# Optimization experiments

Hardware: AMD Instinct MI355X
Metric: run time of the kernel (lower is better)

## Reference

```python
import jax, jax.numpy as jnp
import numpy as np
import math

VOCAB, D, L, H, DFF, S, B = 32000, 1024, 6, 16, 4096, 512, 4
DK = D // H
EPS = 1e-6


def layernorm(x, g, b):
    # Faithful to source: divides by (std + eps), std is population std (unbiased=False)
    mu = jnp.mean(x, axis=-1, keepdims=True)
    std = jnp.sqrt(jnp.mean((x - mu) ** 2, axis=-1, keepdims=True))
    return g * (x - mu) / (std + EPS) + b


def setup_inputs() -> dict:
    key = jax.random.key(0)
    ks = jax.random.split(key, 12)
    s = 0.02
    inp = {
        "tokens": jax.random.randint(ks[0], (B, S), 0, VOCAB, dtype=jnp.int32),
        "tok_emb": jax.random.normal(ks[1], (VOCAB, D), jnp.float32) * s,
        "pos_emb": jax.random.normal(ks[2], (1, S, D), jnp.float32) * s,
        # per-layer stacked params [L, ...]
        "Wq": jax.random.normal(ks[3], (L, D, D), jnp.float32) * s,
        "bq": jnp.zeros((L, D), jnp.float32),
        "Wk": jax.random.normal(ks[4], (L, D, D), jnp.float32) * s,
        "bk": jnp.zeros((L, D), jnp.float32),
        "Wv": jax.random.normal(ks[5], (L, D, D), jnp.float32) * s,
        "bv": jnp.zeros((L, D), jnp.float32),
        "Wo": jax.random.normal(ks[6], (L, D, D), jnp.float32) * s,
        "bo": jnp.zeros((L, D), jnp.float32),
        "g1": jnp.ones((L, D), jnp.float32),
        "be1": jnp.zeros((L, D), jnp.float32),
        "W1": jax.random.normal(ks[7], (L, D, DFF), jnp.float32) * s,
        "bf1": jnp.zeros((L, DFF), jnp.float32),
        "W2": jax.random.normal(ks[8], (L, DFF, D), jnp.float32) * s,
        "bf2": jnp.zeros((L, D), jnp.float32),
        "g2": jnp.ones((L, D), jnp.float32),
        "be2": jnp.zeros((L, D), jnp.float32),
        "gf": jnp.ones((D,), jnp.float32),
        "bf": jnp.zeros((D,), jnp.float32),
    }
    return inp


def gpt_forward(tokens, tok_emb, pos_emb, Wq, bq, Wk, bk, Wv, bv, Wo, bo,
                g1, be1, W1, bf1, W2, bf2, g2, be2, gf, bf):
    seq = tokens.shape[1]
    x = tok_emb[tokens] * math.sqrt(D) + pos_emb[:, :seq, :]  # [B,S,D]
    causal = jnp.tril(jnp.ones((seq, seq), bool))  # [S,S]

    def block(x, p):
        wq, bq_, wk, bk_, wv, bv_, wo, bo_, g1_, be1_, w1, bf1_, w2, bf2_, g2_, be2_ = p
        h = layernorm(x, g1_, be1_)
        q = (h @ wq + bq_).reshape(B, seq, H, DK).transpose(0, 2, 1, 3)  # [B,H,S,DK]
        k = (h @ wk + bk_).reshape(B, seq, H, DK).transpose(0, 2, 1, 3)
        v = (h @ wv + bv_).reshape(B, seq, H, DK).transpose(0, 2, 1, 3)
        scores = jnp.einsum("bhqd,bhkd->bhqk", q, k) / math.sqrt(DK)
        scores = jnp.where(causal, scores, -1e9)
        p_attn = jax.nn.softmax(scores, axis=-1)
        attn = jnp.einsum("bhqk,bhkd->bhqd", p_attn, v)
        attn = attn.transpose(0, 2, 1, 3).reshape(B, seq, D)
        x = x + (attn @ wo + bo_)
        h2 = layernorm(x, g2_, be2_)
        ff = jnp.maximum(h2 @ w1 + bf1_, 0.0) @ w2 + bf2_
        return x + ff, None

    params = (Wq, bq, Wk, bk, Wv, bv, Wo, bo, g1, be1, W1, bf1, W2, bf2, g2, be2)
    x, _ = jax.lax.scan(block, x, params)
    x = layernorm(x, gf, bf)
    logits = x @ tok_emb.T  # tied head, no bias
    return logits


def reference(tokens, tok_emb, pos_emb, Wq, bq, Wk, bk, Wv, bv, Wo, bo,
              g1, be1, W1, bf1, W2, bf2, g2, be2, gf, bf):
    return gpt_forward(tokens, tok_emb, pos_emb, Wq, bq, Wk, bk, Wv, bv, Wo, bo,
                       g1, be1, W1, bf1, W2, bf2, g2, be2, gf, bf)
```

## Files before the change

### kernel.cpp

```cpp
#include <hip/hip_runtime.h>

#define TOKENS 2048
#define DM 1024
#define NHEAD 16
#define DH 64
#define SEQL 512
#define NBATCH 4
#define DFFN 4096
#define NLAYER 6
#define NVOCAB 32000

typedef short short8 __attribute__((ext_vector_type(8)));
typedef short short4v __attribute__((ext_vector_type(4)));
typedef float floatx4 __attribute__((ext_vector_type(4)));

#define FLAG_RELU 1
#define FLAG_OUTBF16 2

#define AS1 __attribute__((address_space(1)))
#define AS3 __attribute__((address_space(3)))

__device__ __forceinline__ float bf2f(short s) {
  unsigned u = ((unsigned)(unsigned short)s) << 16;
  return __builtin_bit_cast(float, u);
}
__device__ __forceinline__ short f2bf(float f) {
  unsigned u = __builtin_bit_cast(unsigned, f);
  u = (u + 0x7FFFu + ((u >> 16) & 1u)) >> 16;
  return (short)(unsigned short)u;
}

template<int N> __device__ __forceinline__ void wait_vm() {
  if constexpr (N == 0)      asm volatile("s_waitcnt vmcnt(0)" ::: "memory");
  else if constexpr (N == 3) asm volatile("s_waitcnt vmcnt(3)" ::: "memory");
  else if constexpr (N == 4) asm volatile("s_waitcnt vmcnt(4)" ::: "memory");
  else if constexpr (N == 6) asm volatile("s_waitcnt vmcnt(6)" ::: "memory");
  else if constexpr (N == 8) asm volatile("s_waitcnt vmcnt(8)" ::: "memory");
  else static_assert(N == 0, "unsupported vmcnt");
}

template<int BM, int BN, int WR, int WC, int BK>
__global__ __launch_bounds__(256) void gemm_db(
    const short* __restrict__ A, const short* __restrict__ Bt, void* __restrict__ Cv,
    const float* __restrict__ bias, const float* __restrict__ resid,
    int K, int lda, int ldb, int ldc, float alpha, int flags)
{
  constexpr int FI = BM / WR / 16;
  constexpr int FJ = BN / WC / 16;
  constexpr int RPI = (BK == 64) ? 32 : 64;
  constexpr int NST = BM / RPI + BN / RPI;
  __shared__ short As[2][BM * BK];
  __shared__ short Bs[2][BN * BK];

  const int gy = gridDim.y;
  int lin = blockIdx.x + gridDim.x * blockIdx.y;
  const int nwg = gridDim.x * gy;
  if ((nwg & 7) == 0) { const int cpx = nwg >> 3; lin = (lin & 7) * cpx + (lin >> 3); }
  const int row0 = (lin % gy) * BM, col0 = (lin / gy) * BN;

  const int tid = threadIdx.x;
  const int lane = tid & 63;
  const int wid = tid >> 6;
  const int wr = wid / WC, wc = wid % WC;
  const int lc = lane & 15, g = lane >> 4;
  const int sr = (BK == 64) ? (tid >> 3) : (tid >> 2);
  const int sc = (BK == 64) ? (tid & 7) : (tid & 3);
  const int swz_s = (BK == 64) ? (sr & 7) : ((sr >> 1) & 3);
  const int scs = (sc ^ swz_s) * 8;

  floatx4 acc[FI][FJ];
  #pragma unroll
  for (int i = 0; i < FI; ++i)
    #pragma unroll
    for (int j = 0; j < FJ; ++j)
      acc[i][j] = (floatx4){0.f, 0.f, 0.f, 0.f};

  auto stage = [&](int k0, int b) {
    char* ad = (char*)As[b];
    char* bd = (char*)Bs[b];
    #pragma unroll
    for (int it = 0; it < BM / RPI; ++it) {
      const short* src = A + (long)(row0 + it * RPI + sr) * lda + k0 + scs;
      __builtin_amdgcn_global_load_lds((const AS1 void*)src,
          (AS3 void*)(ad + it * 4096 + tid * 16), 16, 0, 0);
    }
    #pragma unroll
    for (int it = 0; it < BN / RPI; ++it) {
      const short* src = Bt + (long)(col0 + it * RPI + sr) * ldb + k0 + scs;
      __builtin_amdgcn_global_load_lds((const AS1 void*)src,
          (AS3 void*)(bd + it * 4096 + tid * 16), 16, 0, 0);
    }
  };

  const int NT = K / BK;
  stage(0, 0);
  int cb = 0;
  for (int t = 0; t < NT; ++t) {
    __builtin_amdgcn_s_barrier();
    __builtin_amdgcn_sched_barrier(0);
    if (t + 1 < NT) {
      stage((t + 1) * BK, cb ^ 1);
      wait_vm<NST>();
    } else {
      wait_vm<0>();
    }
    __builtin_amdgcn_sched_barrier(0);

    const short* as = As[cb];
    const short* bs = Bs[cb];
    if constexpr (BK == 64) {
      short8 fa[FI][2], fb[FJ][2];
      #pragma unroll
      for (int i = 0; i < FI; ++i) {
        const int r = wr * (BM / WR) + i * 16 + lc;
        fa[i][0] = *(const short8*)&as[r * 64 + ((g ^ (r & 7)) * 8)];
        fa[i][1] = *(const short8*)&as[r * 64 + (((4 + g) ^ (r & 7)) * 8)];
      }
      #pragma unroll
      for (int j = 0; j < FJ; ++j) {
        const int r = wc * (BN / WC) + j * 16 + lc;
        fb[j][0] = *(const short8*)&bs[r * 64 + ((g ^ (r & 7)) * 8)];
        fb[j][1] = *(const short8*)&bs[r * 64 + (((4 + g) ^ (r & 7)) * 8)];
      }
      #pragma unroll
      for (int i = 0; i < FI; ++i)
        #pragma unroll
        for (int j = 0; j < FJ; ++j) {
          acc[i][j] = __builtin_amdgcn_mfma_f32_16x16x32_bf16(fa[i][0], fb[j][0], acc[i][j], 0, 0, 0);
          acc[i][j] = __builtin_amdgcn_mfma_f32_16x16x32_bf16(fa[i][1], fb[j][1], acc[i][j], 0, 0, 0);
        }
    } else {
      short8 fa[FI], fb[FJ];
      #pragma unroll
      for (int i = 0; i < FI; ++i) {
        const int r = wr * (BM / WR) + i * 16 + lc;
        fa[i] = *(const short8*)&as[r * 32 + ((g ^ ((r >> 1) & 3)) * 8)];
      }
      #pragma unroll
      for (int j = 0; j < FJ; ++j) {
        const int r = wc * (BN / WC) + j * 16 + lc;
        fb[j] = *(const short8*)&bs[r * 32 + ((g ^ ((r >> 1) & 3)) * 8)];
      }
      #pragma unroll
      for (int i = 0; i < FI; ++i)
        #pragma unroll
        for (int j = 0; j < FJ; ++j)
          acc[i][j] = __builtin_amdgcn_mfma_f32_16x16x32_bf16(fa[i], fb[j], acc[i][j], 0, 0, 0);
    }
    cb ^= 1;
  }

  const bool relu = flags & FLAG_RELU;
  const bool obf  = flags & FLAG_OUTBF16;
  float* Cf = (float*)Cv;
  short* Cb = (short*)Cv;
  #pragma unroll
  for (int i = 0; i < FI; ++i) {
    int orow = row0 + wr * (BM / WR) + i * 16 + g * 4;
    #pragma unroll
    for (int j = 0; j < FJ; ++j) {
      int ocol = col0 + wc * (BN / WC) + j * 16 + lc;
      #pragma unroll
      for (int t = 0; t < 4; ++t) {
        long off = (long)(orow + t) * ldc + ocol;
        float v = alpha * acc[i][j][t];
        if (bias)  v += bias[ocol];
        if (resid) v += resid[off];
        if (relu)  v = fmaxf(v, 0.f);
        if (obf) Cb[off] = f2bf(v); else Cf[off] = v;
      }
    }
  }
}

template<int BM, int BN, int WR, int WC, int BK>
static inline void launch_gemm(hipStream_t st, const short* A, const short* Bt, void* C,
    const float* bias, const float* resid, int M, int N, int K,
    int lda, int ldb, int ldc, float alpha, int flags)
{
  dim3 grid(N / BN, M / BM, 1), blk(256);
  gemm_db<BM, BN, WR, WC, BK><<<grid, blk, 0, st>>>(A, Bt, C, bias, resid,
                                                    K, lda, ldb, ldc, alpha, flags);
}

__global__ __launch_bounds__(512, 2) void gemm256h(
    const short* __restrict__ A, const short* __restrict__ Bt, float* __restrict__ C,
    int K, int lda, int ldb, int ldc)
{
  __shared__ short As[2][256 * 32];
  __shared__ short Bs[2][256 * 32];

  const int gy = gridDim.y;
  int lin = blockIdx.x + gridDim.x * blockIdx.y;
  const int nwg = gridDim.x * gy;
  if ((nwg & 7) == 0) { const int cpx = nwg >> 3; lin = (lin & 7) * cpx + (lin >> 3); }
  const int row0 = (lin % gy) * 256, col0 = (lin / gy) * 256;

  const int tid = threadIdx.x;
  const int lane = tid & 63;
  const int w = tid >> 6;
  const int wr = w >> 2, wc = w & 3;
  const int lc = lane & 15, g = lane >> 4;
  const int sr = tid >> 2;
  const int sc = tid & 3;
  const int scs = (sc ^ ((sr >> 1) & 3)) * 8;

  floatx4 acc[8][4];
  #pragma unroll
  for (int i = 0; i < 8; ++i)
    #pragma unroll
    for (int j = 0; j < 4; ++j)
      acc[i][j] = (floatx4){0.f, 0.f, 0.f, 0.f};

  auto stage = [&](int k0, int b) {
    char* ad = (char*)As[b];
    char* bd = (char*)Bs[b];
    #pragma unroll
    for (int it = 0; it < 2; ++it) {
      const short* src = A + (long)(row0 + it * 128 + sr) * lda + k0 + scs;
      __builtin_amdgcn_global_load_lds((const AS1 void*)src,
          (AS3 void*)(ad + it * 8192 + tid * 16), 16, 0, 0);
    }
    #pragma unroll
    for (int it = 0; it < 2; ++it) {
      const short* src = Bt + (long)(col0 + it * 128 + sr) * ldb + k0 + scs;
      __builtin_amdgcn_global_load_lds((const AS1 void*)src,
          (AS3 void*)(bd + it * 8192 + tid * 16), 16, 0, 0);
    }
  };

  const int NT = K >> 5;
  stage(0, 0);
  int cb = 0;
  for (int t = 0; t < NT; ++t) {
    __builtin_amdgcn_s_barrier();
    __builtin_amdgcn_sched_barrier(0);
    if (t + 1 < NT) {
      stage((t + 1) << 5, cb ^ 1);
      wait_vm<4>();
    } else {
      wait_vm<0>();
    }
    __builtin_amdgcn_sched_barrier(0);

    const short* as = As[cb];
    const short* bs = Bs[cb];
    short8 fa[8], fb[4];
    #pragma unroll
    for (int i = 0; i < 8; ++i) {
      const int r = wr * 128 + i * 16 + lc;
      fa[i] = *(const short8*)&as[r * 32 + ((g ^ ((r >> 1) & 3)) * 8)];
    }
    #pragma unroll
    for (int j = 0; j < 4; ++j) {
      const int r = wc * 64 + j * 16 + lc;
      fb[j] = *(const short8*)&bs[r * 32 + ((g ^ ((r >> 1) & 3)) * 8)];
    }
    #pragma unroll
    for (int i = 0; i < 8; ++i)
      #pragma unroll
      for (int j = 0; j < 4; ++j)
        acc[i][j] = __builtin_amdgcn_mfma_f32_16x16x32_bf16(fa[i], fb[j], acc[i][j], 0, 0, 0);
    cb ^= 1;
  }

  #pragma unroll
  for (int i = 0; i < 8; ++i) {
    int orow = row0 + wr * 128 + i * 16 + g * 4;
    #pragma unroll
    for (int j = 0; j < 4; ++j) {
      int ocol = col0 + wc * 64 + j * 16 + lc;
      #pragma unroll
      for (int t = 0; t < 4; ++t)
        C[(long)(orow + t) * ldc + ocol] = acc[i][j][t];
    }
  }
}

__global__ __launch_bounds__(256) void flash_attn(
    const short* __restrict__ qkv, const short* __restrict__ Vt,
    short* __restrict__ attn)
{
  const int qt = blockIdx.x;
  const int bh = blockIdx.y;
  const int b = bh >> 4, h = bh & 15;
  const int row0 = qt * 64;

  __shared__ short Kt[64 * 64];
  __shared__ short Vtl[64 * 64];
  __shared__ short Pt[4 * 16 * 64];

  const int tid = threadIdx.x;
  const int lane = tid & 63;
  const int wid = tid >> 6;
  const int lc = lane & 15, g = lane >> 4;

  short8 qf[2];
  {
    const short* qp = qkv + (long)(b * SEQL + row0 + wid * 16 + lc) * 3072 + h * DH;
    qf[0] = *(const short8*)(qp + g * 8);
    qf[1] = *(const short8*)(qp + 32 + g * 8);
  }

  floatx4 o[4];
  float m[4], l[4];
  #pragma unroll
  for (int j = 0; j < 4; ++j) o[j] = (floatx4){0.f, 0.f, 0.f, 0.f};
  #pragma unroll
  for (int t = 0; t < 4; ++t) { m[t] = -3e38f; l[t] = 0.f; }

  for (int kv0 = 0; kv0 <= row0; kv0 += 64) {
    #pragma unroll
    for (int i = 0; i < 2; ++i) {
      const int idx = i * 256 + tid;
      const int r = idx >> 3, cc = idx & 7;
      const int sw = cc ^ (r & 7);
      const short* ks = qkv + (long)(b * SEQL + kv0 + r) * 3072 + 1024 + h * DH + sw * 8;
      __builtin_amdgcn_global_load_lds((const AS1 void*)ks,
          (AS3 void*)((char*)Kt + (i * 256 + wid * 64) * 16), 16, 0, 0);
      const short* vs = Vt + (long)bh * DH * SEQL + (long)r * SEQL + kv0 + sw * 8;
      __builtin_amdgcn_global_load_lds((const AS1 void*)vs,
          (AS3 void*)((char*)Vtl + (i * 256 + wid * 64) * 16), 16, 0, 0);
    }
    __syncthreads();

    floatx4 s[4];
    #pragma unroll
    for (int j = 0; j < 4; ++j) s[j] = (floatx4){0.f, 0.f, 0.f, 0.f};
    #pragma unroll
    for (int ks_ = 0; ks_ < 2; ++ks_) {
      #pragma unroll
      for (int j = 0; j < 4; ++j) {
        const int row = j * 16 + lc;
        const short8 kf = *(const short8*)&Kt[row * 64 + ((ks_ * 4 + g) ^ (row & 7)) * 8];
        s[j] = __builtin_amdgcn_mfma_f32_16x16x32_bf16(qf[ks_], kf, s[j], 0, 0, 0);
      }
    }

    const bool diag = (kv0 == row0);
    float p[4][4], rmax[4], rsum[4], fs[4];
    #pragma unroll
    for (int t = 0; t < 4; ++t) rmax[t] = -3e38f;
    #pragma unroll
    for (int j = 0; j < 4; ++j)
      #pragma unroll
      for (int t = 0; t < 4; ++t) {
        float sv = s[j][t] * 0.125f;
        if (diag && (j * 16 + lc) > (wid * 16 + g * 4 + t)) sv = -3e38f;
        p[j][t] = sv;
        rmax[t] = fmaxf(rmax[t], sv);
      }
    #pragma unroll
    for (int t = 0; t < 4; ++t) {
      #pragma unroll
      for (int mk = 1; mk < 16; mk <<= 1)
        rmax[t] = fmaxf(rmax[t], __shfl_xor(rmax[t], mk));
      float mn = fmaxf(m[t], rmax[t]);
      fs[t] = __expf(m[t] - mn);
      m[t] = mn;
    }
    #pragma unroll
    for (int j = 0; j < 4; ++j)
      #pragma unroll
      for (int t = 0; t < 4; ++t)
        p[j][t] = __expf(p[j][t] - m[t]);
    #pragma unroll
    for (int t = 0; t < 4; ++t) {
      rsum[t] = p[0][t] + p[1][t] + p[2][t] + p[3][t];
      #pragma unroll
      for (int mk = 1; mk < 16; mk <<= 1)
        rsum[t] += __shfl_xor(rsum[t], mk);
      l[t] = l[t] * fs[t] + rsum[t];
    }
    #pragma unroll
    for (int j = 0; j < 4; ++j) {
      o[j][0] *= fs[0]; o[j][1] *= fs[1]; o[j][2] *= fs[2]; o[j][3] *= fs[3];
    }
    #pragma unroll
    for (int j = 0; j < 4; ++j)
      #pragma unroll
      for (int t = 0; t < 4; ++t) {
        const int r = g * 4 + t;
        const int col = j * 16 + lc;
        Pt[wid * 1024 + r * 64 + (((col >> 3) ^ (r & 7)) * 8) + (col & 7)] = f2bf(p[j][t]);
      }
    __syncthreads();

    #pragma unroll
    for (int ks_ = 0; ks_ < 2; ++ks_) {
      const short8 pf = *(const short8*)&Pt[wid * 1024 + lc * 64 + ((ks_ * 4 + g) ^ (lc & 7)) * 8];
      #pragma unroll
      for (int j = 0; j < 4; ++j) {
        const int row = j * 16 + lc;
        const short8 vf = *(const short8*)&Vtl[row * 64 + ((ks_ * 4 + g) ^ (row & 7)) * 8];
        o[j] = __builtin_amdgcn_mfma_f32_16x16x32_bf16(pf, vf, o[j], 0, 0, 0);
      }
    }
    __syncthreads();
  }

  float linv[4];
  #pragma unroll
  for (int t = 0; t < 4; ++t) linv[t] = 1.f / l[t];
  #pragma unroll
  for (int j = 0; j < 4; ++j)
    #pragma unroll
    for (int t = 0; t < 4; ++t) {
      const long row = (long)(b * SEQL + row0 + wid * 16 + g * 4 + t);
      attn[row * DM + h * DH + j * 16 + lc] = f2bf(o[j][t] * linv[t]);
    }
}

__global__ __launch_bounds__(256) void ln_bf16(const float* __restrict__ x,
    const float* __restrict__ gg, const float* __restrict__ bb, short* __restrict__ out)
{
  int row = blockIdx.x;
  const float4 u = ((const float4*)(x + (long)row * DM))[threadIdx.x];
  float s  = u.x + u.y + u.z + u.w;
  float sq = u.x * u.x + u.y * u.y + u.z * u.z + u.w * u.w;
  #pragma unroll
  for (int o = 32; o; o >>= 1) { s += __shfl_xor(s, o); sq += __shfl_xor(sq, o); }
  __shared__ float red[8];
  int lane = threadIdx.x & 63, wid = threadIdx.x >> 6;
  if (lane == 0) { red[wid] = s; red[4 + wid] = sq; }
  __syncthreads();
  s  = red[0] + red[1] + red[2] + red[3];
  sq = red[4] + red[5] + red[6] + red[7];
  float mu  = s * (1.f / DM);
  float var = fmaxf(sq * (1.f / DM) - mu * mu, 0.f);
  float inv = 1.f / (sqrtf(var) + 1e-6f);
  int c = threadIdx.x * 4;
  const float4 gv = ((const float4*)gg)[threadIdx.x];
  const float4 bv = ((const float4*)bb)[threadIdx.x];
  short4v o;
  o[0] = f2bf((u.x - mu) * inv * gv.x + bv.x);
  o[1] = f2bf((u.y - mu) * inv * gv.y + bv.y);
  o[2] = f2bf((u.z - mu) * inv * gv.z + bv.z);
  o[3] = f2bf((u.w - mu) * inv * gv.w + bv.w);
  *(short4v*)(out + (long)row * DM + c) = o;
}

__global__ __launch_bounds__(256) void embed_k(const int* __restrict__ toks,
    const float* __restrict__ emb, const float* __restrict__ pos, float* __restrict__ x)
{
  int row = blockIdx.x;
  int s = row & (SEQL - 1);
  long tk = toks[row];
  const float4 e = ((const float4*)(emb + tk * DM))[threadIdx.x];
  const float4 p = ((const float4*)(pos + (long)s * DM))[threadIdx.x];
  float4 o;
  o.x = e.x * 32.f + p.x; o.y = e.y * 32.f + p.y;
  o.z = e.z * 32.f + p.z; o.w = e.w * 32.f + p.w;
  ((float4*)(x + (long)row * DM))[threadIdx.x] = o;
}

__global__ void wtrans(const float* __restrict__ W, short* __restrict__ Wt,
                       int K, int N, long zsout)
{
  __shared__ float tile[32][33];
  const long lo = (long)blockIdx.z * K * N;
  const long oo = (long)blockIdx.z * zsout;
  int n0 = blockIdx.x * 32, k0 = blockIdx.y * 32;
  int tx = threadIdx.x, ty = threadIdx.y;
  #pragma unroll
  for (int i = 0; i < 4; ++i)
    tile[ty + i * 8][tx] = W[lo + (long)(k0 + ty + i * 8) * N + n0 + tx];
  __syncthreads();
  #pragma unroll
  for (int i = 0; i < 4; ++i)
    Wt[oo + (long)(n0 + ty + i * 8) * K + k0 + tx] = f2bf(tile[tx][ty + i * 8]);
}

__global__ __launch_bounds__(256) void conv_bf16(const float* __restrict__ in,
                                                 short* __restrict__ out)
{
  long i = ((long)blockIdx.x * 256 + threadIdx.x) * 8;
  float4 a = *(const float4*)(in + i);
  float4 b = *(const float4*)(in + i + 4);
  short8 o;
  o[0] = f2bf(a.x); o[1] = f2bf(a.y); o[2] = f2bf(a.z); o[3] = f2bf(a.w);
  o[4] = f2bf(b.x); o[5] = f2bf(b.y); o[6] = f2bf(b.z); o[7] = f2bf(b.w);
  *(short8*)(out + i) = o;
}

__global__ void vtrans(const short* __restrict__ qkv, short* __restrict__ Vt)
{
  __shared__ short tile[32][33];
  int bh = blockIdx.z;
  int b = bh >> 4, h = bh & 15;
  int s0 = blockIdx.x * 32, d0 = blockIdx.y * 32;
  int tx = threadIdx.x, ty = threadIdx.y;
  #pragma unroll
  for (int i = 0; i < 4; ++i)
    tile[ty + i * 8][tx] =
        qkv[((long)(b * SEQL + s0 + ty + i * 8)) * 3072 + 2048 + h * DH + d0 + tx];
  __syncthreads();
  #pragma unroll
  for (int i = 0; i < 4; ++i)
    Vt[((long)(bh * DH + d0 + ty + i * 8)) * SEQL + s0 + tx] = tile[tx][ty + i * 8];
}

__global__ void bias_cat(const float* __restrict__ bq, const float* __restrict__ bk,
                         const float* __restrict__ bv, float* __restrict__ out)
{
  int l = blockIdx.y;
  int i = blockIdx.x * 256 + threadIdx.x;
  float v = (i < 1024) ? bq[l * 1024 + i]
          : (i < 2048) ? bk[l * 1024 + i - 1024]
                       : bv[l * 1024 + i - 2048];
  out[(long)l * 3072 + i] = v;
}

extern "C" void kernel_launch(void* const* d_in, const int* in_sizes, int n_in,
                              void* d_out, int out_size, void* d_ws, size_t ws_size,
                              hipStream_t stream)
{
  (void)in_sizes; (void)n_in; (void)out_size;
  const int*   toks = (const int*)  d_in[0];
  const float* temb = (const float*)d_in[1];
  const float* pemb = (const float*)d_in[2];
  const float* Wq  = (const float*)d_in[3];  const float* bq  = (const float*)d_in[4];
  const float* Wk  = (const float*)d_in[5];  const float* bk  = (const float*)d_in[6];
  const float* Wv  = (const float*)d_in[7];  const float* bv  = (const float*)d_in[8];
  const float* Wo  = (const float*)d_in[9];  const float* bo  = (const float*)d_in[10];
  const float* g1  = (const float*)d_in[11]; const float* be1 = (const float*)d_in[12];
  const float* W1  = (const float*)d_in[13]; const float* bf1 = (const float*)d_in[14];
  const float* W2  = (const float*)d_in[15]; const float* bf2 = (const float*)d_in[16];
  const float* g2  = (const float*)d_in[17]; const float* be2 = (const float*)d_in[18];
  const float* gf  = (const float*)d_in[19]; const float* bfb = (const float*)d_in[20];

  char* p = (char*)d_ws;
  auto carve = [&](size_t bytes) -> char* {
    char* r = p;
    p += (bytes + 255) & ~(size_t)255;
    return r;
  };
  short* h     = (short*)carve((size_t)TOKENS * DM * 2);
  char*  uni   = p;
  short* tembb = (short*)uni;
  short* Wqkvt = (short*)carve((size_t)NLAYER * 3072 * DM * 2);
  short* Wot   = (short*)carve((size_t)NLAYER * DM * DM * 2);
  short* W1t   = (short*)carve((size_t)NLAYER * DM * DFFN * 2);
  short* W2t   = (short*)carve((size_t)NLAYER * DM * DFFN * 2);
  float* x     = (float*)carve((size_t)TOKENS * DM * 4);
  short* qkv   = (short*)carve((size_t)TOKENS * 3072 * 2);
  short* attn  = (short*)carve((size_t)TOKENS * DM * 2);
  short* Vt    = (short*)carve((size_t)NBATCH * NHEAD * DH * SEQL * 2);
  short* ffb   = (short*)carve((size_t)TOKENS * DFFN * 2);
  float* bqkv  = (float*)carve((size_t)NLAYER * 3072 * 4);
  size_t used = (size_t)(p - (char*)d_ws);
  size_t need_t = (size_t)(uni - (char*)d_ws) + (size_t)NVOCAB * DM * 2;
  if (used > ws_size || need_t > ws_size) return;

  dim3 tb(32, 8);

  embed_k<<<TOKENS, 256, 0, stream>>>(toks, temb, pemb, x);
  bias_cat<<<dim3(12, NLAYER), 256, 0, stream>>>(bq, bk, bv, bqkv);
  wtrans<<<dim3(DM / 32, DM / 32, NLAYER), tb, 0, stream>>>(Wq, Wqkvt, DM, DM, 3072L * DM);
  wtrans<<<dim3(DM / 32, DM / 32, NLAYER), tb, 0, stream>>>(Wk, Wqkvt + (size_t)DM * DM, DM, DM, 3072L * DM);
  wtrans<<<dim3(DM / 32, DM / 32, NLAYER), tb, 0, stream>>>(Wv, Wqkvt + (size_t)2 * DM * DM, DM, DM, 3072L * DM);
  wtrans<<<dim3(DM / 32, DM / 32, NLAYER), tb, 0, stream>>>(Wo, Wot, DM, DM, (long)DM * DM);
  wtrans<<<dim3(DFFN / 32, DM / 32, NLAYER), tb, 0, stream>>>(W1, W1t, DM, DFFN, (long)DM * DFFN);
  wtrans<<<dim3(DM / 32, DFFN / 32, NLAYER), tb, 0, stream>>>(W2, W2t, DFFN, DM, (long)DM * DFFN);

  for (int l = 0; l < NLAYER; ++l) {
    const size_t wqkv = (size_t)l * 3072 * DM;
    const size_t wdd  = (size_t)l * DM * DM;
    const size_t wdf  = (size_t)l * DM * DFFN;
    ln_bf16<<<TOKENS, 256, 0, stream>>>(x, g1 + l * DM, be1 + l * DM, h);
    launch_gemm<128, 128, 2, 2, 64>(stream, h, Wqkvt + wqkv, qkv, bqkv + (size_t)l * 3072,
        nullptr, TOKENS, 3072, DM, DM, DM, 3072, 1.f, FLAG_OUTBF16);
    vtrans<<<dim3(SEQL / 32, DH / 32, NBATCH * NHEAD), tb, 0, stream>>>(qkv, Vt);
    flash_attn<<<dim3(SEQL / 64, NBATCH * NHEAD), 256, 0, stream>>>(qkv, Vt, attn);
    launch_gemm<64, 128, 1, 4, 64>(stream, attn, Wot + wdd, x, bo + l * DM, x,
        TOKENS, DM, DM, DM, DM, DM, 1.f, 0);
    ln_bf16<<<TOKENS, 256, 0, stream>>>(x, g2 + l * DM, be2 + l * DM, h);
    launch_gemm<128, 128, 2, 2, 64>(stream, h, W1t + wdf, ffb, bf1 + l * DFFN, nullptr,
        TOKENS, DFFN, DM, DM, DM, DFFN, 1.f, FLAG_OUTBF16 | FLAG_RELU);
    launch_gemm<64, 128, 1, 4, 64>(stream, ffb, W2t + wdf, x, bf2 + l * DM, x,
        TOKENS, DM, DFFN, DFFN, DFFN, DM, 1.f, 0);
  }
  ln_bf16<<<TOKENS, 256, 0, stream>>>(x, gf, bfb, h);
  conv_bf16<<<(NVOCAB * DM) / (256 * 8), 256, 0, stream>>>(temb, tembb);
  {
    dim3 grid(NVOCAB / 256, TOKENS / 256, 1), blk(512);
    gemm256h<<<grid, blk, 0, stream>>>(h, tembb, (float*)d_out, DM, DM, DM, NVOCAB);
  }
}
```

Measured before the change: 1.557 ms.

## Restructure vocab-head GEMM into ping-pong phased pipeline with BK=64

Rewrites the 256x256 logits GEMM kernel to use a K-tile of 64 split into quarter and half sub-tiles. Each iteration runs in four phases that interleave LDS fragment reads, staged global-to-LDS loads of the next B and next-next A tiles, and MFMA bursts. The phases are separated by barriers and s_setprio, in the style of a ping-pong schedule. The aim is to overlap memory traffic with MFMA work and halve the loop trip count. In exchange it adds more barriers per iteration and a larger LDS footprint (128KB), which could limit occupancy.

```diff
diff --git a/kernel.cpp b/kernel.cpp
--- a/kernel.cpp
+++ b/kernel.cpp
@@ -183,12 +183,12 @@
                                                     K, lda, ldb, ldc, alpha, flags);
 }
 
-__global__ __launch_bounds__(512, 2) void gemm256h(
+__global__ __launch_bounds__(512, 2) void gemm256p(
     const short* __restrict__ A, const short* __restrict__ Bt, float* __restrict__ C,
     int K, int lda, int ldb, int ldc)
 {
-  __shared__ short As[2][256 * 32];
-  __shared__ short Bs[2][256 * 32];
+  __shared__ short As[2][2][128 * 64];
+  __shared__ short Bs[2][4][64 * 64];
 
   const int gy = gridDim.y;
   int lin = blockIdx.x + gridDim.x * blockIdx.y;
@@ -201,9 +201,9 @@
   const int w = tid >> 6;
   const int wr = w >> 2, wc = w & 3;
   const int lc = lane & 15, g = lane >> 4;
-  const int sr = tid >> 2;
-  const int sc = tid & 3;
-  const int scs = (sc ^ ((sr >> 1) & 3)) * 8;
+  const int sr = tid >> 3;
+  const int sc = tid & 7;
+  const int scs = (sc ^ (sr & 7)) * 8;
 
   floatx4 acc[8][4];
   #pragma unroll
@@ -212,57 +212,98 @@
     for (int j = 0; j < 4; ++j)
       acc[i][j] = (floatx4){0.f, 0.f, 0.f, 0.f};
 
-  auto stage = [&](int k0, int b) {
-    char* ad = (char*)As[b];
-    char* bd = (char*)Bs[b];
+  auto stageA = [&](int k0, int b, int h) {
     #pragma unroll
     for (int it = 0; it < 2; ++it) {
-      const short* src = A + (long)(row0 + it * 128 + sr) * lda + k0 + scs;
+      const int r = h * 128 + it * 64 + sr;
+      const short* src = A + (long)(row0 + r) * lda + k0 + scs;
       __builtin_amdgcn_global_load_lds((const AS1 void*)src,
-          (AS3 void*)(ad + it * 8192 + tid * 16), 16, 0, 0);
-    }
-    #pragma unroll
-    for (int it = 0; it < 2; ++it) {
-      const short* src = Bt + (long)(col0 + it * 128 + sr) * ldb + k0 + scs;
-      __builtin_amdgcn_global_load_lds((const AS1 void*)src,
-          (AS3 void*)(bd + it * 8192 + tid * 16), 16, 0, 0);
+          (AS3 void*)((char*)&As[b][h][0] + it * 8192 + tid * 16), 16, 0, 0);
     }
   };
-
-  const int NT = K >> 5;
-  stage(0, 0);
-  int cb = 0;
+  auto stageBq = [&](int k0, int b, int q) {
+    const short* src = Bt + (long)(col0 + q * 64 + sr) * ldb + k0 + scs;
+    __builtin_amdgcn_global_load_lds((const AS1 void*)src,
+        (AS3 void*)((char*)&Bs[b][q][0] + tid * 16), 16, 0, 0);
+  };
+  auto rdA = [&](int b, int sub, short8 fa[4][2]) {
+    const short* base = &As[b][wr][0];
+    #pragma unroll
+    for (int i = 0; i < 4; ++i) {
+      const int r = sub * 64 + i * 16 + lc;
+      fa[i][0] = *(const short8*)&base[r * 64 + ((g ^ (r & 7)) * 8)];
+      fa[i][1] = *(const short8*)&base[r * 64 + (((4 + g) ^ (r & 7)) * 8)];
+    }
+  };
+  auto rdB = [&](int b, int sub, short8 fb[2][2]) {
+    const short* base = &Bs[b][wc][0];
+    #pragma unroll
+    for (int j = 0; j < 2; ++j) {
+      const int r = sub * 32 + j * 16 + lc;
+      fb[j][0] = *(const short8*)&base[r * 64 + ((g ^ (r & 7)) * 8)];
+      fb[j][1] = *(const short8*)&base[r * 64 + (((4 + g) ^ (r & 7)) * 8)];
+    }
+  };
+  auto mm = [&](short8 fa[4][2], short8 fb[2][2], int io, int jo) {
+    #pragma unroll
+    for (int i = 0; i < 4; ++i)
+      #pragma unroll
+      for (int j = 0; j < 2; ++j) {
+        floatx4 c = acc[io + i][jo + j];
+        c = __builtin_amdgcn_mfma_f32_16x16x32_bf16(fa[i][0], fb[j][0], c, 0, 0, 0);
+        c = __builtin_amdgcn_mfma_f32_16x16x32_bf16(fa[i][1], fb[j][1], c, 0, 0, 0);
+        acc[io + i][jo + j] = c;
+      }
+  };
+
+#define PH_SYNC() \
+    __builtin_amdgcn_s_barrier(); \
+    asm volatile("s_waitcnt lgkmcnt(0)" ::: "memory"); \
+    __builtin_amdgcn_sched_barrier(0); \
+    __builtin_amdgcn_s_setprio(1);
+#define PH_END() \
+    __builtin_amdgcn_s_setprio(0); \
+    __builtin_amdgcn_s_barrier();
+
+  const int NT = K >> 6;
+  stageA(0, 0, 0); stageA(0, 0, 1);
+  stageBq(0, 0, 0); stageBq(0, 0, 1); stageBq(0, 0, 2); stageBq(0, 0, 3);
+  stageA(64, 1, 0); stageA(64, 1, 1);
+  wait_vm<4>();
+  __builtin_amdgcn_s_barrier();
+
   for (int t = 0; t < NT; ++t) {
-    __builtin_amdgcn_s_barrier();
-    __builtin_amdgcn_sched_barrier(0);
-    if (t + 1 < NT) {
-      stage((t + 1) << 5, cb ^ 1);
+    const int b = t & 1;
+    const int nk = (t + 1) << 6;
+    short8 fa[4][2], fb0[2][2], fb1[2][2];
+    rdA(b, 0, fa); rdB(b, 0, fb0);
+    if (t + 1 < NT) { stageBq(nk, b ^ 1, 0); stageBq(nk, b ^ 1, 1); }
+    PH_SYNC();
+    mm(fa, fb0, 0, 0);
+    PH_END();
+    rdB(b, 1, fb1);
+    if (t + 1 < NT) { stageBq(nk, b ^ 1, 2); stageBq(nk, b ^ 1, 3); }
+    PH_SYNC();
+    mm(fa, fb1, 0, 2);
+    PH_END();
+    rdA(b, 1, fa);
+    PH_SYNC();
+    mm(fa, fb1, 4, 2);
+    PH_END();
+    if (t + 2 < NT) {
+      stageA((t + 2) << 6, b, 0); stageA((t + 2) << 6, b, 1);
       wait_vm<4>();
     } else {
       wait_vm<0>();
     }
     __builtin_amdgcn_sched_barrier(0);
-
-    const short* as = As[cb];
-    const short* bs = Bs[cb];
-    short8 fa[8], fb[4];
-    #pragma unroll
-    for (int i = 0; i < 8; ++i) {
-      const int r = wr * 128 + i * 16 + lc;
-      fa[i] = *(const short8*)&as[r * 32 + ((g ^ ((r >> 1) & 3)) * 8)];
-    }
-    #pragma unroll
-    for (int j = 0; j < 4; ++j) {
-      const int r = wc * 64 + j * 16 + lc;
-      fb[j] = *(const short8*)&bs[r * 32 + ((g ^ ((r >> 1) & 3)) * 8)];
-    }
-    #pragma unroll
-    for (int i = 0; i < 8; ++i)
-      #pragma unroll
-      for (int j = 0; j < 4; ++j)
-        acc[i][j] = __builtin_amdgcn_mfma_f32_16x16x32_bf16(fa[i], fb[j], acc[i][j], 0, 0, 0);
-    cb ^= 1;
-  }
+    __builtin_amdgcn_s_barrier();
+    __builtin_amdgcn_s_setprio(1);
+    mm(fa, fb0, 4, 0);
+    PH_END();
+  }
+#undef PH_SYNC
+#undef PH_END
 
   #pragma unroll
   for (int i = 0; i < 8; ++i) {
@@ -584,6 +625,6 @@
   conv_bf16<<<(NVOCAB * DM) / (256 * 8), 256, 0, stream>>>(temb, tembb);
   {
     dim3 grid(NVOCAB / 256, TOKENS / 256, 1), blk(512);
-    gemm256h<<<grid, blk, 0, stream>>>(h, tembb, (float*)d_out, DM, DM, DM, NVOCAB);
-  }
-}
+    gemm256p<<<grid, blk, 0, stream>>>(h, tembb, (float*)d_out, DM, DM, DM, NVOCAB);
+  }
+}
```

New measurement: 1.532 ms. About the same (-1.6%).
